# Optimization experiments

Hardware: AMD Instinct MI355X
Metric: run time of the kernel (lower is better)

The kernel has to match this reference:

```python
import jax, jax.numpy as jnp
import numpy as np

B, N, C, NH = 4, 2304, 256, 8
HD = C // NH            # head dim = 32
HS = WS = 48            # H = W = sqrt(N)
RADIUS = 3.0
MLP_HID = 4 * C
SCALE = HD ** (-0.5)
NEG = -1e9              # stands in for -inf (identical softmax up to fp eps)
EPS = 1e-6


def spatial_mask():
    # get_spatial_mask: cdist of (y, x) grid coords, -inf where dist > radius
    yy, xx = jnp.meshgrid(jnp.arange(HS), jnp.arange(WS), indexing='ij')
    coords = jnp.stack([yy, xx], -1).reshape(-1, 2).astype(jnp.float32)  # [N, 2]
    d2 = jnp.sum((coords[:, None, :] - coords[None, :, :]) ** 2, -1)     # [N, N]
    return jnp.where(d2 > RADIUS * RADIUS, NEG, 0.0)


def layernorm(x, g, b):
    mu = jnp.mean(x, -1, keepdims=True)
    var = jnp.mean((x - mu) ** 2, -1, keepdims=True)
    return (x - mu) * jax.lax.rsqrt(var + EPS) * g + b


def setup_inputs() -> dict:
    key = jax.random.key(0)
    ks = jax.random.split(key, 16)
    s = 0.02
    return {
        'x':    jax.random.normal(ks[0], (B, N, C), jnp.float32),
        'x_kv': jax.random.normal(ks[1], (B, N, C), jnp.float32),
        'Wq': jax.random.normal(ks[2], (C, C), jnp.float32) * s,
        'bq': jnp.zeros((C,), jnp.float32),
        'Wk': jax.random.normal(ks[3], (C, C), jnp.float32) * s,
        'bk': jnp.zeros((C,), jnp.float32),
        'Wv': jax.random.normal(ks[4], (C, C), jnp.float32) * s,
        'bv': jnp.zeros((C,), jnp.float32),
        'Wp': jax.random.normal(ks[5], (C, C), jnp.float32) * s,
        'bp': jnp.zeros((C,), jnp.float32),
        'g1': jnp.ones((C,), jnp.float32),
        'b1': jnp.zeros((C,), jnp.float32),
        'g2': jnp.ones((C,), jnp.float32),
        'b2': jnp.zeros((C,), jnp.float32),
        'W1': jax.random.normal(ks[6], (C, MLP_HID), jnp.float32) * s,
        'bm1': jnp.zeros((MLP_HID,), jnp.float32),
        'W2': jax.random.normal(ks[7], (MLP_HID, C), jnp.float32) * s,
        'bm2': jnp.zeros((C,), jnp.float32),
    }


def reference(x, x_kv, Wq, bq, Wk, bk, Wv, bv, Wp, bp,
              g1, b1, g2, b2, W1, bm1, W2, bm2):
    mask = spatial_mask()                                  # [N, N]
    h = layernorm(x, g1, b1)
    hkv = layernorm(x_kv, g1, b1)
    q = (h @ Wq + bq).reshape(B, N, NH, HD)
    k = (hkv @ Wk + bk).reshape(B, N, NH, HD)
    v = (hkv @ Wv + bv).reshape(B, N, NH, HD)
    scores = jnp.einsum('bqhd,bkhd->bhqk', q, k) * SCALE + mask
    attn = jax.nn.softmax(scores, axis=-1)
    out = jnp.einsum('bhqk,bkhd->bqhd', attn, v).reshape(B, N, C)
    x = x + out @ Wp + bp
    m = layernorm(x, g2, b2)
    x = x + jax.nn.gelu(m @ W1 + bm1, approximate=False) @ W2 + bm2
    return x
```

## Files before the change

### kernel.cpp

```cpp
#include <hip/hip_runtime.h>
#include <hip/hip_fp16.h>
#include <math.h>

#define BB 4
#define NN 2304
#define CC 256
#define HS 48
#define HID 1024
#define BNROWS (BB * NN)
#define ATTN_SCALE 0.17677669529663687f

typedef _Float16 f16;
typedef __attribute__((ext_vector_type(2))) _Float16 h2;
typedef __attribute__((ext_vector_type(8))) _Float16 h8;
typedef __attribute__((ext_vector_type(4))) float f4;

static __device__ __forceinline__ float block_sum256(float v) {
    __shared__ float sh[4];
    v += __shfl_down(v, 32, 64);
    v += __shfl_down(v, 16, 64);
    v += __shfl_down(v, 8, 64);
    v += __shfl_down(v, 4, 64);
    v += __shfl_down(v, 2, 64);
    v += __shfl_down(v, 1, 64);
    const int lane = threadIdx.x & 63;
    const int wid = threadIdx.x >> 6;
    if (lane == 0) sh[wid] = v;
    __syncthreads();
    float r = sh[0] + sh[1] + sh[2] + sh[3];
    __syncthreads();
    return r;
}

__global__ __launch_bounds__(256) void prep_kernel(
    const float* __restrict__ Wq, const float* __restrict__ Wk,
    const float* __restrict__ Wv, const float* __restrict__ Wp,
    const float* __restrict__ W1, const float* __restrict__ W2,
    f16* __restrict__ WqT, f16* __restrict__ WkvT, f16* __restrict__ WpT,
    f16* __restrict__ W1T, f16* __restrict__ W2T)
{
    __shared__ float t[32][33];
    int bx = blockIdx.x;
    const float* src; f16* dst; int K, N;
    if (bx < 64)        { src = Wq; dst = WqT;               K = 256;  N = 256; }
    else if (bx < 128)  { src = Wk; dst = WkvT;              K = 256;  N = 256;  bx -= 64; }
    else if (bx < 192)  { src = Wv; dst = WkvT + 256 * 256;  K = 256;  N = 256;  bx -= 128; }
    else if (bx < 256)  { src = Wp; dst = WpT;               K = 256;  N = 256;  bx -= 192; }
    else if (bx < 512)  { src = W1; dst = W1T;               K = 256;  N = 1024; bx -= 256; }
    else                { src = W2; dst = W2T;               K = 1024; N = 256;  bx -= 512; }
    const int tN = N >> 5;
    const int kt = bx / tN, nt = bx - kt * tN;
    const int rr = threadIdx.x >> 5, cc = threadIdx.x & 31;
#pragma unroll
    for (int j = 0; j < 4; ++j)
        t[rr + 8 * j][cc] = src[(size_t)(kt * 32 + rr + 8 * j) * N + nt * 32 + cc];
    __syncthreads();
#pragma unroll
    for (int j = 0; j < 4; ++j)
        dst[(size_t)(nt * 32 + rr + 8 * j) * K + kt * 32 + cc] = (f16)t[cc][rr + 8 * j];
}

__global__ __launch_bounds__(256) void ln_dual_kernel(
    const float* __restrict__ x, const float* __restrict__ xkv,
    const float* __restrict__ g, const float* __restrict__ be,
    f16* __restrict__ h, f16* __restrict__ hkv)
{
    const int row = blockIdx.x;
    const float* src;
    f16* dst;
    if (row < BNROWS) { src = x + (size_t)row * CC;              dst = h + (size_t)row * CC; }
    else              { src = xkv + (size_t)(row - BNROWS) * CC; dst = hkv + (size_t)(row - BNROWS) * CC; }
    const int t = threadIdx.x;
    const float v = src[t];
    const float mu = block_sum256(v) * (1.0f / CC);
    const float d = v - mu;
    const float var = block_sum256(d * d) * (1.0f / CC);
    const float r = rsqrtf(var + 1e-6f);
    dst[t] = (f16)(d * r * g[t] + be[t]);
}

__global__ __launch_bounds__(256) void ln_single_kernel(
    const float* __restrict__ src, const float* __restrict__ g,
    const float* __restrict__ be, f16* __restrict__ dst)
{
    const int row = blockIdx.x;
    const int t = threadIdx.x;
    const float v = src[(size_t)row * CC + t];
    const float mu = block_sum256(v) * (1.0f / CC);
    const float d = v - mu;
    const float var = block_sum256(d * d) * (1.0f / CC);
    const float r = rsqrtf(var + 1e-6f);
    dst[(size_t)row * CC + t] = (f16)(d * r * g[t] + be[t]);
}

template <bool GELU, int RESID, int OUTF32, bool DUALB>
__global__ __launch_bounds__(256) void gemm_f16(
    const f16* __restrict__ A, const f16* __restrict__ Bt,
    const float* __restrict__ bias, const float* __restrict__ bias2,
    const float* __restrict__ resid, void* __restrict__ outp,
    int M, int N, int K)
{
    __shared__ f16 As[128][40];
    __shared__ f16 Bs[64][40];
    const int tid = threadIdx.x;
    const int wid = tid >> 6, lane = tid & 63;
    const int ln15 = lane & 15, quad = lane >> 4;
    const int m0 = blockIdx.y * 128, n0 = blockIdx.x * 64;

    const int ar0 = tid >> 2, ak0 = (tid & 3) << 3;
    const int ar1 = (tid + 256) >> 2, ak1 = ak0;
    const int bn = tid >> 2, bk = (tid & 3) << 3;

    f4 acc[2][4];
#pragma unroll
    for (int i = 0; i < 2; ++i)
#pragma unroll
        for (int j = 0; j < 4; ++j) acc[i][j] = (f4){0.f, 0.f, 0.f, 0.f};

    for (int k0 = 0; k0 < K; k0 += 32) {
        *(uint4*)&As[ar0][ak0] = *(const uint4*)&A[(size_t)(m0 + ar0) * K + k0 + ak0];
        *(uint4*)&As[ar1][ak1] = *(const uint4*)&A[(size_t)(m0 + ar1) * K + k0 + ak1];
        *(uint4*)&Bs[bn][bk]   = *(const uint4*)&Bt[(size_t)(n0 + bn) * K + k0 + bk];
        __syncthreads();
        h8 bF[4], aF[2];
#pragma unroll
        for (int nt = 0; nt < 4; ++nt)
            bF[nt] = *(const h8*)&Bs[nt * 16 + ln15][quad * 8];
#pragma unroll
        for (int mt = 0; mt < 2; ++mt)
            aF[mt] = *(const h8*)&As[wid * 32 + mt * 16 + ln15][quad * 8];
#pragma unroll
        for (int mt = 0; mt < 2; ++mt)
#pragma unroll
            for (int nt = 0; nt < 4; ++nt)
                acc[mt][nt] = __builtin_amdgcn_mfma_f32_16x16x32_f16(
                    aF[mt], bF[nt], acc[mt][nt], 0, 0, 0);
        __syncthreads();
    }

#pragma unroll
    for (int nt = 0; nt < 4; ++nt) {
        const int gn = n0 + nt * 16 + ln15;
        const float bs = DUALB ? (gn < 256 ? bias[gn] : bias2[gn - 256]) : bias[gn];
#pragma unroll
        for (int mt = 0; mt < 2; ++mt) {
#pragma unroll
            for (int r = 0; r < 4; ++r) {
                const int gm = m0 + wid * 32 + mt * 16 + quad * 4 + r;
                float v = acc[mt][nt][r] + bs;
                if (GELU) v = 0.5f * v * (1.0f + erff(v * 0.70710678118654752f));
                if (RESID) v += resid[(size_t)gm * N + gn];
                if (OUTF32) ((float*)outp)[(size_t)gm * N + gn] = v;
                else ((f16*)outp)[(size_t)gm * N + gn] = (f16)v;
            }
        }
    }
}

__device__ __constant__ int ATT_DY[29] = {
    -3, -2, -2, -2, -2, -2, -1, -1, -1, -1, -1, 0, 0, 0, 0,
    0, 0, 0, 1, 1, 1, 1, 1, 2, 2, 2, 2, 2, 3};
__device__ __constant__ int ATT_DX[29] = {
    0, -2, -1, 0, 1, 2, -2, -1, 0, 1, 2, -3, -2, -1, 0,
    1, 2, 3, -2, -1, 0, 1, 2, -2, -1, 0, 1, 2, 0};

__global__ __launch_bounds__(128) void attn_tile_kernel(
    const f16* __restrict__ qf, const f16* __restrict__ kvf,
    f16* __restrict__ ao)
{
    __shared__ f16 ks[196][66];
    __shared__ f16 vs[196][66];
    const int tile = blockIdx.x, hp = blockIdx.y, b = blockIdx.z;
    const int ty0 = (tile / 6) * 8, tx0 = (tile - (tile / 6) * 6) * 8;
    const int tid = threadIdx.x;

    for (int idx = tid; idx < 196 * 16; idx += 128) {
        const int r = idx >> 4, seg = idx & 15;
        const int gy = ty0 - 3 + r / 14, gx = tx0 - 3 + (r - (r / 14) * 14);
        uint4 val = {0u, 0u, 0u, 0u};
        if ((unsigned)gy < HS && (unsigned)gx < HS) {
            const size_t rowb = ((size_t)b * NN + gy * HS + gx) * 512;
            const int ch = (seg < 8) ? (hp * 64 + seg * 8)
                                     : (256 + hp * 64 + (seg - 8) * 8);
            val = *(const uint4*)&kvf[rowb + ch];
        }
        f16* dstp = (seg < 8) ? &ks[r][(seg & 7) * 8] : &vs[r][(seg & 7) * 8];
        ((unsigned int*)dstp)[0] = val.x;
        ((unsigned int*)dstp)[1] = val.y;
        ((unsigned int*)dstp)[2] = val.z;
        ((unsigned int*)dstp)[3] = val.w;
    }
    __syncthreads();

    const int q = tid & 63, hh = tid >> 6;
    const int qy = q >> 3, qx = q & 7;
    const size_t qrow = (size_t)b * NN + (ty0 + qy) * HS + tx0 + qx;
    const f16* qp = qf + qrow * CC + hp * 64 + hh * 32;
    uint4 qa[4];
#pragma unroll
    for (int i = 0; i < 4; ++i) qa[i] = ((const uint4*)qp)[i];
    const h2* q2 = (const h2*)qa;

    float s[29];
#pragma unroll
    for (int n = 0; n < 29; ++n) {
        const int dy = ATT_DY[n], dx = ATT_DX[n];
        const int r = (qy + 3 + dy) * 14 + qx + 3 + dx;
        const bool valid = (unsigned)(ty0 + qy + dy) < HS &&
                           (unsigned)(tx0 + qx + dx) < HS;
        float a = 0.0f;
        const h2* kp = (const h2*)&ks[r][hh * 32];
#pragma unroll
        for (int i = 0; i < 16; ++i)
            a = __builtin_amdgcn_fdot2(q2[i], kp[i], a, false);
        s[n] = valid ? a * ATTN_SCALE : -1e30f;
    }
    float m = s[0];
#pragma unroll
    for (int n = 1; n < 29; ++n) m = fmaxf(m, s[n]);
    float l = 0.0f;
#pragma unroll
    for (int n = 0; n < 29; ++n) { s[n] = __expf(s[n] - m); l += s[n]; }
    h2 a2[16];
#pragma unroll
    for (int i = 0; i < 16; ++i) a2[i] = (h2){(f16)0.f, (f16)0.f};
#pragma unroll
    for (int n = 0; n < 29; ++n) {
        const int dy = ATT_DY[n], dx = ATT_DX[n];
        const int r = (qy + 3 + dy) * 14 + qx + 3 + dx;
        const f16 pn = (f16)s[n];
        const h2 ph = (h2){pn, pn};
        const h2* vp = (const h2*)&vs[r][hh * 32];
#pragma unroll
        for (int i = 0; i < 16; ++i) a2[i] += ph * vp[i];
    }
    const float inv = 1.0f / l;
    uint4 ov[4];
    f16* oh = (f16*)ov;
#pragma unroll
    for (int i = 0; i < 16; ++i) {
        oh[2 * i]     = (f16)((float)a2[i][0] * inv);
        oh[2 * i + 1] = (f16)((float)a2[i][1] * inv);
    }
    uint4* dst = (uint4*)(ao + qrow * CC + hp * 64 + hh * 32);
#pragma unroll
    for (int i = 0; i < 4; ++i) dst[i] = ov[i];
}

extern "C" void kernel_launch(void* const* d_in, const int* in_sizes, int n_in,
                              void* d_out, int out_size, void* d_ws, size_t ws_size,
                              hipStream_t stream) {
    const float* x    = (const float*)d_in[0];
    const float* x_kv = (const float*)d_in[1];
    const float* Wq   = (const float*)d_in[2];
    const float* bq   = (const float*)d_in[3];
    const float* Wk   = (const float*)d_in[4];
    const float* bk   = (const float*)d_in[5];
    const float* Wv   = (const float*)d_in[6];
    const float* bv   = (const float*)d_in[7];
    const float* Wp   = (const float*)d_in[8];
    const float* bp   = (const float*)d_in[9];
    const float* g1   = (const float*)d_in[10];
    const float* b1   = (const float*)d_in[11];
    const float* g2   = (const float*)d_in[12];
    const float* b2   = (const float*)d_in[13];
    const float* W1   = (const float*)d_in[14];
    const float* bm1  = (const float*)d_in[15];
    const float* W2   = (const float*)d_in[16];
    const float* bm2  = (const float*)d_in[17];
    float* outp = (float*)d_out;

    f16* wsh = (f16*)d_ws;
    f16* WqT  = wsh;
    f16* WkvT = wsh + 65536;
    f16* WpT  = wsh + 196608;
    f16* W1T  = wsh + 262144;
    f16* W2T  = wsh + 524288;
    f16* hq   = wsh + 786432;
    f16* hkv  = wsh + 3145728;
    f16* qf   = wsh + 5505024;
    f16* kvf  = wsh + 7864320;
    f16* ao   = hq;
    float* x1 = (float*)(wsh + 3145728);
    f16* m2   = kvf;
    f16* hidF = wsh + 12582912;
    f16* hidB = wsh + 10223616;
    const bool fused = ws_size >= (size_t)22020096 * sizeof(f16);

    prep_kernel<<<768, 256, 0, stream>>>(Wq, Wk, Wv, Wp, W1, W2,
                                         WqT, WkvT, WpT, W1T, W2T);
    ln_dual_kernel<<<2 * BNROWS, 256, 0, stream>>>(x, x_kv, g1, b1, hq, hkv);
    gemm_f16<false, 0, 0, false><<<dim3(4, 72), 256, 0, stream>>>(
        hq, WqT, bq, nullptr, nullptr, qf, BNROWS, CC, CC);
    gemm_f16<false, 0, 0, true><<<dim3(8, 72), 256, 0, stream>>>(
        hkv, WkvT, bk, bv, nullptr, kvf, BNROWS, 512, CC);
    attn_tile_kernel<<<dim3(36, 4, BB), 128, 0, stream>>>(qf, kvf, ao);
    gemm_f16<false, 1, 1, false><<<dim3(4, 72), 256, 0, stream>>>(
        ao, WpT, bp, nullptr, x, x1, BNROWS, CC, CC);
    ln_single_kernel<<<BNROWS, 256, 0, stream>>>(x1, g2, b2, m2);
    if (fused) {
        gemm_f16<true, 0, 0, false><<<dim3(16, 72), 256, 0, stream>>>(
            m2, W1T, bm1, nullptr, nullptr, hidF, BNROWS, HID, CC);
        gemm_f16<false, 1, 1, false><<<dim3(4, 72), 256, 0, stream>>>(
            hidF, W2T, bm2, nullptr, x1, outp, BNROWS, CC, HID);
    } else {
        for (int b = 0; b < BB; ++b) {
            const size_t off = (size_t)b * NN * CC;
            gemm_f16<true, 0, 0, false><<<dim3(16, 18), 256, 0, stream>>>(
                m2 + off, W1T, bm1, nullptr, nullptr, hidB, NN, HID, CC);
            gemm_f16<false, 1, 1, false><<<dim3(4, 18), 256, 0, stream>>>(
                hidB, W2T, bm2, nullptr, x1 + off, outp + off, NN, CC, HID);
        }
    }
    (void)in_sizes; (void)n_in; (void)out_size;
}
```

Measured before the change: 210.7 us.

## Merge QKV GEMMs, use wave-per-row layernorm, 64x64 GEMM tiles, f16 residual

Q and KV projections are fused into one GEMM launch over a concatenated weight and bias. The layernorm kernels now give each row to one wave, using float4 loads and xor shuffles with no block barriers. The GEMM tile changes from 128x64 with BK32 to 64x64 with BK64, and the x1 intermediate is stored in f16 to cut traffic. These changes reduce launch count, synchronisation and memory bandwidth, at the cost of some precision in the residual stream.

Result: faster. 200.1 us (-5.0%).

```diff
diff --git a/kernel.cpp b/kernel.cpp
--- a/kernel.cpp
+++ b/kernel.cpp
@@ -15,36 +15,38 @@
 typedef __attribute__((ext_vector_type(8))) _Float16 h8;
 typedef __attribute__((ext_vector_type(4))) float f4;
 
-static __device__ __forceinline__ float block_sum256(float v) {
-    __shared__ float sh[4];
-    v += __shfl_down(v, 32, 64);
-    v += __shfl_down(v, 16, 64);
-    v += __shfl_down(v, 8, 64);
-    v += __shfl_down(v, 4, 64);
-    v += __shfl_down(v, 2, 64);
-    v += __shfl_down(v, 1, 64);
-    const int lane = threadIdx.x & 63;
-    const int wid = threadIdx.x >> 6;
-    if (lane == 0) sh[wid] = v;
-    __syncthreads();
-    float r = sh[0] + sh[1] + sh[2] + sh[3];
-    __syncthreads();
-    return r;
+static __device__ __forceinline__ float wave_sum64(float v) {
+    v += __shfl_xor(v, 32, 64);
+    v += __shfl_xor(v, 16, 64);
+    v += __shfl_xor(v, 8, 64);
+    v += __shfl_xor(v, 4, 64);
+    v += __shfl_xor(v, 2, 64);
+    v += __shfl_xor(v, 1, 64);
+    return v;
 }
 
 __global__ __launch_bounds__(256) void prep_kernel(
     const float* __restrict__ Wq, const float* __restrict__ Wk,
     const float* __restrict__ Wv, const float* __restrict__ Wp,
     const float* __restrict__ W1, const float* __restrict__ W2,
-    f16* __restrict__ WqT, f16* __restrict__ WkvT, f16* __restrict__ WpT,
-    f16* __restrict__ W1T, f16* __restrict__ W2T)
-{
-    __shared__ float t[32][33];
+    const float* __restrict__ bq, const float* __restrict__ bk,
+    const float* __restrict__ bv,
+    f16* __restrict__ WqkvT, f16* __restrict__ WpT,
+    f16* __restrict__ W1T, f16* __restrict__ W2T, float* __restrict__ bqkv)
+{
     int bx = blockIdx.x;
+    if (bx == 768) {
+        const int t = threadIdx.x;
+        bqkv[t]       = bq[t];
+        bqkv[t + 256] = bk[t];
+        bqkv[t + 512] = bv[t];
+        return;
+    }
+    __shared__ float tt[32][33];
     const float* src; f16* dst; int K, N;
-    if (bx < 64)        { src = Wq; dst = WqT;               K = 256;  N = 256; }
-    else if (bx < 128)  { src = Wk; dst = WkvT;              K = 256;  N = 256;  bx -= 64; }
-    else if (bx < 192)  { src = Wv; dst = WkvT + 256 * 256;  K = 256;  N = 256;  bx -= 128; }
+    if (bx < 64)        { src = Wq; dst = WqkvT;             K = 256;  N = 256; }
+    else if (bx < 128)  { src = Wk; dst = WqkvT + 65536;     K = 256;  N = 256;  bx -= 64; }
+    else if (bx < 192)  { src = Wv; dst = WqkvT + 131072;    K = 256;  N = 256;  bx -= 128; }
     else if (bx < 256)  { src = Wp; dst = WpT;               K = 256;  N = 256;  bx -= 192; }
     else if (bx < 512)  { src = W1; dst = W1T;               K = 256;  N = 1024; bx -= 256; }
     else                { src = W2; dst = W2T;               K = 1024; N = 256;  bx -= 512; }
@@ -53,105 +55,122 @@
     const int rr = threadIdx.x >> 5, cc = threadIdx.x & 31;
 #pragma unroll
     for (int j = 0; j < 4; ++j)
-        t[rr + 8 * j][cc] = src[(size_t)(kt * 32 + rr + 8 * j) * N + nt * 32 + cc];
+        tt[rr + 8 * j][cc] = src[(size_t)(kt * 32 + rr + 8 * j) * N + nt * 32 + cc];
     __syncthreads();
 #pragma unroll
     for (int j = 0; j < 4; ++j)
-        dst[(size_t)(nt * 32 + rr + 8 * j) * K + kt * 32 + cc] = (f16)t[cc][rr + 8 * j];
-}
-
-__global__ __launch_bounds__(256) void ln_dual_kernel(
+        dst[(size_t)(nt * 32 + rr + 8 * j) * K + kt * 32 + cc] = (f16)tt[cc][rr + 8 * j];
+}
+
+__global__ __launch_bounds__(256) void ln1_kernel(
     const float* __restrict__ x, const float* __restrict__ xkv,
     const float* __restrict__ g, const float* __restrict__ be,
-    f16* __restrict__ h, f16* __restrict__ hkv)
-{
-    const int row = blockIdx.x;
-    const float* src;
-    f16* dst;
-    if (row < BNROWS) { src = x + (size_t)row * CC;              dst = h + (size_t)row * CC; }
-    else              { src = xkv + (size_t)(row - BNROWS) * CC; dst = hkv + (size_t)(row - BNROWS) * CC; }
-    const int t = threadIdx.x;
-    const float v = src[t];
-    const float mu = block_sum256(v) * (1.0f / CC);
-    const float d = v - mu;
-    const float var = block_sum256(d * d) * (1.0f / CC);
-    const float r = rsqrtf(var + 1e-6f);
-    dst[t] = (f16)(d * r * g[t] + be[t]);
-}
-
-__global__ __launch_bounds__(256) void ln_single_kernel(
-    const float* __restrict__ src, const float* __restrict__ g,
-    const float* __restrict__ be, f16* __restrict__ dst)
-{
-    const int row = blockIdx.x;
-    const int t = threadIdx.x;
-    const float v = src[(size_t)row * CC + t];
-    const float mu = block_sum256(v) * (1.0f / CC);
-    const float d = v - mu;
-    const float var = block_sum256(d * d) * (1.0f / CC);
-    const float r = rsqrtf(var + 1e-6f);
-    dst[(size_t)row * CC + t] = (f16)(d * r * g[t] + be[t]);
-}
-
-template <bool GELU, int RESID, int OUTF32, bool DUALB>
-__global__ __launch_bounds__(256) void gemm_f16(
-    const f16* __restrict__ A, const f16* __restrict__ Bt,
-    const float* __restrict__ bias, const float* __restrict__ bias2,
-    const float* __restrict__ resid, void* __restrict__ outp,
-    int M, int N, int K)
-{
-    __shared__ f16 As[128][40];
-    __shared__ f16 Bs[64][40];
+    f16* __restrict__ hq, f16* __restrict__ hkv)
+{
+    const int r = blockIdx.x * 4 + (threadIdx.x >> 6);
+    const int lane = threadIdx.x & 63;
+    const float* src; f16* dst;
+    if (r < BNROWS) { src = x + (size_t)r * CC;             dst = hq + (size_t)r * CC; }
+    else { src = xkv + (size_t)(r - BNROWS) * CC; dst = hkv + (size_t)(r - BNROWS) * CC; }
+    const float4 v = ((const float4*)src)[lane];
+    const float mu = wave_sum64(v.x + v.y + v.z + v.w) * (1.0f / CC);
+    const float d0 = v.x - mu, d1 = v.y - mu, d2 = v.z - mu, d3 = v.w - mu;
+    const float var = wave_sum64(d0 * d0 + d1 * d1 + d2 * d2 + d3 * d3) * (1.0f / CC);
+    const float rs = rsqrtf(var + 1e-6f);
+    const float4 g4 = ((const float4*)g)[lane];
+    const float4 b4 = ((const float4*)be)[lane];
+    h2 o01 = (h2){(f16)(d0 * rs * g4.x + b4.x), (f16)(d1 * rs * g4.y + b4.y)};
+    h2 o23 = (h2){(f16)(d2 * rs * g4.z + b4.z), (f16)(d3 * rs * g4.w + b4.w)};
+    ((h2*)dst)[lane * 2] = o01;
+    ((h2*)dst)[lane * 2 + 1] = o23;
+}
+
+__global__ __launch_bounds__(256) void ln2_kernel(
+    const f16* __restrict__ x1, const float* __restrict__ g,
+    const float* __restrict__ be, f16* __restrict__ m2)
+{
+    const int r = blockIdx.x * 4 + (threadIdx.x >> 6);
+    const int lane = threadIdx.x & 63;
+    const f16* src = x1 + (size_t)r * CC;
+    const h2 a01 = ((const h2*)src)[lane * 2];
+    const h2 a23 = ((const h2*)src)[lane * 2 + 1];
+    const float v0 = (float)a01[0], v1 = (float)a01[1];
+    const float v2 = (float)a23[0], v3 = (float)a23[1];
+    const float mu = wave_sum64(v0 + v1 + v2 + v3) * (1.0f / CC);
+    const float d0 = v0 - mu, d1 = v1 - mu, d2 = v2 - mu, d3 = v3 - mu;
+    const float var = wave_sum64(d0 * d0 + d1 * d1 + d2 * d2 + d3 * d3) * (1.0f / CC);
+    const float rs = rsqrtf(var + 1e-6f);
+    const float4 g4 = ((const float4*)g)[lane];
+    const float4 b4 = ((const float4*)be)[lane];
+    f16* dst = m2 + (size_t)r * CC;
+    h2 o01 = (h2){(f16)(d0 * rs * g4.x + b4.x), (f16)(d1 * rs * g4.y + b4.y)};
+    h2 o23 = (h2){(f16)(d2 * rs * g4.z + b4.z), (f16)(d3 * rs * g4.w + b4.w)};
+    ((h2*)dst)[lane * 2] = o01;
+    ((h2*)dst)[lane * 2 + 1] = o23;
+}
+
+template <bool GELU, int RESID, bool OUTF32, bool QKV>
+__global__ __launch_bounds__(256) void gemm64(
+    const f16* __restrict__ Aq, const f16* __restrict__ Akv,
+    const f16* __restrict__ Bt, const float* __restrict__ bias,
+    const void* __restrict__ resid, void* __restrict__ out1,
+    void* __restrict__ outkv, int M, int N, int K)
+{
+    __shared__ f16 As[64][72];
+    __shared__ f16 Bs[64][72];
     const int tid = threadIdx.x;
     const int wid = tid >> 6, lane = tid & 63;
     const int ln15 = lane & 15, quad = lane >> 4;
-    const int m0 = blockIdx.y * 128, n0 = blockIdx.x * 64;
-
-    const int ar0 = tid >> 2, ak0 = (tid & 3) << 3;
-    const int ar1 = (tid + 256) >> 2, ak1 = ak0;
-    const int bn = tid >> 2, bk = (tid & 3) << 3;
-
-    f4 acc[2][4];
-#pragma unroll
-    for (int i = 0; i < 2; ++i)
-#pragma unroll
-        for (int j = 0; j < 4; ++j) acc[i][j] = (f4){0.f, 0.f, 0.f, 0.f};
-
-    for (int k0 = 0; k0 < K; k0 += 32) {
-        *(uint4*)&As[ar0][ak0] = *(const uint4*)&A[(size_t)(m0 + ar0) * K + k0 + ak0];
-        *(uint4*)&As[ar1][ak1] = *(const uint4*)&A[(size_t)(m0 + ar1) * K + k0 + ak1];
-        *(uint4*)&Bs[bn][bk]   = *(const uint4*)&Bt[(size_t)(n0 + bn) * K + k0 + bk];
+    const int m0 = blockIdx.y * 64;
+    const int n0 = blockIdx.x * 64;
+    const bool kv = QKV && (n0 >= 256);
+    const f16* Ap = (QKV && kv) ? Akv : Aq;
+
+    const int sr = tid >> 2;
+    const int sk = (tid & 3) << 4;
+
+    f4 acc[4];
+#pragma unroll
+    for (int i = 0; i < 4; ++i) acc[i] = (f4){0.f, 0.f, 0.f, 0.f};
+
+    for (int k0 = 0; k0 < K; k0 += 64) {
+        const f16* ag = Ap + (size_t)(m0 + sr) * K + k0 + sk;
+        const f16* bg = Bt + (size_t)(n0 + sr) * K + k0 + sk;
+        *(uint4*)&As[sr][sk]     = *(const uint4*)ag;
+        *(uint4*)&As[sr][sk + 8] = *(const uint4*)(ag + 8);
+        *(uint4*)&Bs[sr][sk]     = *(const uint4*)bg;
+        *(uint4*)&Bs[sr][sk + 8] = *(const uint4*)(bg + 8);
         __syncthreads();
-        h8 bF[4], aF[2];
-#pragma unroll
-        for (int nt = 0; nt < 4; ++nt)
-            bF[nt] = *(const h8*)&Bs[nt * 16 + ln15][quad * 8];
-#pragma unroll
-        for (int mt = 0; mt < 2; ++mt)
-            aF[mt] = *(const h8*)&As[wid * 32 + mt * 16 + ln15][quad * 8];
-#pragma unroll
-        for (int mt = 0; mt < 2; ++mt)
-#pragma unroll
-            for (int nt = 0; nt < 4; ++nt)
-                acc[mt][nt] = __builtin_amdgcn_mfma_f32_16x16x32_f16(
-                    aF[mt], bF[nt], acc[mt][nt], 0, 0, 0);
+#pragma unroll
+        for (int kh = 0; kh < 2; ++kh) {
+            const h8 bF = *(const h8*)&Bs[wid * 16 + ln15][kh * 32 + quad * 8];
+#pragma unroll
+            for (int mt = 0; mt < 4; ++mt) {
+                const h8 aF = *(const h8*)&As[mt * 16 + ln15][kh * 32 + quad * 8];
+                acc[mt] = __builtin_amdgcn_mfma_f32_16x16x32_f16(aF, bF, acc[mt], 0, 0, 0);
+            }
+        }
         __syncthreads();
     }
 
-#pragma unroll
-    for (int nt = 0; nt < 4; ++nt) {
-        const int gn = n0 + nt * 16 + ln15;
-        const float bs = DUALB ? (gn < 256 ? bias[gn] : bias2[gn - 256]) : bias[gn];
-#pragma unroll
-        for (int mt = 0; mt < 2; ++mt) {
-#pragma unroll
-            for (int r = 0; r < 4; ++r) {
-                const int gm = m0 + wid * 32 + mt * 16 + quad * 4 + r;
-                float v = acc[mt][nt][r] + bs;
-                if (GELU) v = 0.5f * v * (1.0f + erff(v * 0.70710678118654752f));
-                if (RESID) v += resid[(size_t)gm * N + gn];
-                if (OUTF32) ((float*)outp)[(size_t)gm * N + gn] = v;
-                else ((f16*)outp)[(size_t)gm * N + gn] = (f16)v;
+    const int gn = n0 + wid * 16 + ln15;
+    const float bs = bias[gn];
+#pragma unroll
+    for (int mt = 0; mt < 4; ++mt) {
+#pragma unroll
+        for (int r = 0; r < 4; ++r) {
+            const int gm = m0 + mt * 16 + quad * 4 + r;
+            float v = acc[mt][r] + bs;
+            if (GELU) v = 0.5f * v * (1.0f + erff(v * 0.70710678118654752f));
+            if (RESID == 1) v += ((const float*)resid)[(size_t)gm * N + gn];
+            if (RESID == 2) v += (float)((const f16*)resid)[(size_t)gm * N + gn];
+            if (QKV) {
+                if (kv) ((f16*)outkv)[(size_t)gm * 512 + (gn - 256)] = (f16)v;
+                else    ((f16*)out1)[(size_t)gm * 256 + gn] = (f16)v;
+            } else if (OUTF32) {
+                ((float*)out1)[(size_t)gm * N + gn] = v;
+            } else {
+                ((f16*)out1)[(size_t)gm * N + gn] = (f16)v;
             }
         }
     }
@@ -271,45 +290,42 @@
     float* outp = (float*)d_out;
 
     f16* wsh = (f16*)d_ws;
-    f16* WqT  = wsh;
-    f16* WkvT = wsh + 65536;
-    f16* WpT  = wsh + 196608;
-    f16* W1T  = wsh + 262144;
-    f16* W2T  = wsh + 524288;
-    f16* hq   = wsh + 786432;
-    f16* hkv  = wsh + 3145728;
-    f16* qf   = wsh + 5505024;
-    f16* kvf  = wsh + 7864320;
-    f16* ao   = hq;
-    float* x1 = (float*)(wsh + 3145728);
-    f16* m2   = kvf;
-    f16* hidF = wsh + 12582912;
-    f16* hidB = wsh + 10223616;
-    const bool fused = ws_size >= (size_t)22020096 * sizeof(f16);
-
-    prep_kernel<<<768, 256, 0, stream>>>(Wq, Wk, Wv, Wp, W1, W2,
-                                         WqT, WkvT, WpT, W1T, W2T);
-    ln_dual_kernel<<<2 * BNROWS, 256, 0, stream>>>(x, x_kv, g1, b1, hq, hkv);
-    gemm_f16<false, 0, 0, false><<<dim3(4, 72), 256, 0, stream>>>(
-        hq, WqT, bq, nullptr, nullptr, qf, BNROWS, CC, CC);
-    gemm_f16<false, 0, 0, true><<<dim3(8, 72), 256, 0, stream>>>(
-        hkv, WkvT, bk, bv, nullptr, kvf, BNROWS, 512, CC);
+    f16* WqkvT = wsh;
+    f16* WpT   = wsh + 196608;
+    f16* W1T   = wsh + 262144;
+    f16* W2T   = wsh + 524288;
+    float* bqkv = (float*)(wsh + 786432);
+    f16* hq    = wsh + 787968;
+    f16* hkv   = wsh + 3147264;
+    f16* qf    = wsh + 5506560;
+    f16* kvf   = wsh + 7865856;
+    f16* ao    = hq;
+    f16* x1    = hkv;
+    f16* m2    = qf;
+    f16* hidF  = kvf;
+    const bool fused = ws_size >= (size_t)17303040 * sizeof(f16);
+
+    prep_kernel<<<769, 256, 0, stream>>>(Wq, Wk, Wv, Wp, W1, W2, bq, bk, bv,
+                                         WqkvT, WpT, W1T, W2T, bqkv);
+    ln1_kernel<<<2 * BNROWS / 4, 256, 0, stream>>>(x, x_kv, g1, b1, hq, hkv);
+    gemm64<false, 0, false, true><<<dim3(12, 144), 256, 0, stream>>>(
+        hq, hkv, WqkvT, bqkv, nullptr, qf, kvf, BNROWS, 768, CC);
     attn_tile_kernel<<<dim3(36, 4, BB), 128, 0, stream>>>(qf, kvf, ao);
-    gemm_f16<false, 1, 1, false><<<dim3(4, 72), 256, 0, stream>>>(
-        ao, WpT, bp, nullptr, x, x1, BNROWS, CC, CC);
-    ln_single_kernel<<<BNROWS, 256, 0, stream>>>(x1, g2, b2, m2);
+    gemm64<false, 1, false, false><<<dim3(4, 144), 256, 0, stream>>>(
+        ao, nullptr, WpT, bp, x, x1, nullptr, BNROWS, CC, CC);
+    ln2_kernel<<<BNROWS / 4, 256, 0, stream>>>(x1, g2, b2, m2);
     if (fused) {
-        gemm_f16<true, 0, 0, false><<<dim3(16, 72), 256, 0, stream>>>(
-            m2, W1T, bm1, nullptr, nullptr, hidF, BNROWS, HID, CC);
-        gemm_f16<false, 1, 1, false><<<dim3(4, 72), 256, 0, stream>>>(
-            hidF, W2T, bm2, nullptr, x1, outp, BNROWS, CC, HID);
+        gemm64<true, 0, false, false><<<dim3(16, 144), 256, 0, stream>>>(
+            m2, nullptr, W1T, bm1, nullptr, hidF, nullptr, BNROWS, HID, CC);
+        gemm64<false, 2, true, false><<<dim3(4, 144), 256, 0, stream>>>(
+            hidF, nullptr, W2T, bm2, x1, outp, nullptr, BNROWS, CC, HID);
     } else {
         for (int b = 0; b < BB; ++b) {
             const size_t off = (size_t)b * NN * CC;
-            gemm_f16<true, 0, 0, false><<<dim3(16, 18), 256, 0, stream>>>(
-                m2 + off, W1T, bm1, nullptr, nullptr, hidB, NN, HID, CC);
-            gemm_f16<false, 1, 1, false><<<dim3(4, 18), 256, 0, stream>>>(
-                hidB, W2T, bm2, nullptr, x1 + off, outp + off, NN, CC, HID);
+            gemm64<true, 0, false, false><<<dim3(16, 36), 256, 0, stream>>>(
+                m2 + off, nullptr, W1T, bm1, nullptr, hidF, nullptr, NN, HID, CC);
+            gemm64<false, 2, true, false><<<dim3(4, 36), 256, 0, stream>>>(
+                hidF, nullptr, W2T, bm2, x1 + off, outp + off, nullptr, NN, CC, HID);
         }
     }
     (void)in_sizes; (void)n_in; (void)out_size;
```
